# Performance work log

Measured on AMD Instinct MI355X. Metric: run time of the kernel, lower is better.

The kernel has to match this reference:

```python
import jax, jax.numpy as jnp
import numpy as np

B, T, C = 4, 4096, 1024   # batch, seq_len, n_embd
HS = 128                  # tamanho_cabeca (head size)


def setup_inputs() -> dict:
    key = jax.random.key(0)
    kx, kq, kk, kv = jax.random.split(key, 4)
    scale = 0.02
    return {
        "x": jax.random.normal(kx, (B, T, C), dtype=jnp.float32),
        "Wq": jax.random.normal(kq, (C, HS), dtype=jnp.float32) * scale,
        "Wk": jax.random.normal(kk, (C, HS), dtype=jnp.float32) * scale,
        "Wv": jax.random.normal(kv, (C, HS), dtype=jnp.float32) * scale,
    }


def reference(x, Wq, Wk, Wv):
    # Single-head causal self-attention, faithful to the torch Head module.
    _, Tn, Cn = x.shape
    q = jnp.einsum("btc,ch->bth", x, Wq)
    k = jnp.einsum("btc,ch->bth", x, Wk)
    v = jnp.einsum("btc,ch->bth", x, Wv)
    # NOTE: original scales by C**-0.5 (input embed dim), not head_size**-0.5.
    scores = jnp.einsum("bth,bsh->bts", q, k) * (Cn ** -0.5)
    causal = jnp.tril(jnp.ones((Tn, Tn), dtype=bool))  # [T, T]
    scores = jnp.where(causal, scores, -jnp.inf)
    probs = jax.nn.softmax(scores, axis=-1)
    return jnp.einsum("bts,bsh->bth", probs, v)
```

## Files before the change

kernel.cpp:

```cpp
#include <hip/hip_runtime.h>
#include <hip/hip_bf16.h>
#include <math.h>

typedef __attribute__((ext_vector_type(8))) short short8;
typedef __attribute__((ext_vector_type(4))) float f32x4;
typedef unsigned short ushort_t;

#define B_  4
#define T_  4096
#define C_  1024
#define HS_ 128

#define QSCALE 0.04508422002778011f

__device__ const unsigned char NS_[32] = {
    1,1,1,1,2,2,3,3,3,4,4,4,5,5,5,6,6,7,7,7,8,8,8,9,9,9,10,10,11,11,11,11};

__device__ __forceinline__ ushort_t f2bf(float f) {
    unsigned int u = __float_as_uint(f);
    u = (u + 0x7FFFu + ((u >> 16) & 1u)) >> 16;
    return (ushort_t)u;
}
__device__ __forceinline__ ushort_t f2bf_fast(float f) {
    return (ushort_t)((__float_as_uint(f) + 0x8000u) >> 16);
}
__device__ __forceinline__ float bf2f(ushort_t u) {
    return __uint_as_float(((unsigned)u) << 16);
}
__device__ __forceinline__ void async16(const void* g, void* l) {
    __builtin_amdgcn_global_load_lds(
        (const __attribute__((address_space(1))) unsigned int*)g,
        (__attribute__((address_space(3))) unsigned int*)l, 16, 0, 0);
}
__device__ __forceinline__ float exp2fast(float x) {
    return __builtin_amdgcn_exp2f(x);
}

__global__ __launch_bounds__(256) void wt_kernel(
    const float* __restrict__ Wq, const float* __restrict__ Wk,
    const float* __restrict__ Wv, ushort_t* __restrict__ WT3)
{
    __shared__ ushort_t sWT[128 * 68];
    const int blk = blockIdx.x, tid = threadIdx.x;
    const int m = blk >> 4, slab = blk & 15;
    const float* __restrict__ W = (m == 0) ? Wq : (m == 1) ? Wk : Wv;
    const int kc = slab * 64;
    const int r = tid >> 2, h0 = (tid & 3) * 32;
#pragma unroll
    for (int j = 0; j < 8; ++j) {
        float4 wv = *(const float4*)(W + (size_t)(kc + r) * 128 + h0 + j * 4);
        sWT[(h0 + j * 4 + 0) * 68 + r] = f2bf(wv.x);
        sWT[(h0 + j * 4 + 1) * 68 + r] = f2bf(wv.y);
        sWT[(h0 + j * 4 + 2) * 68 + r] = f2bf(wv.z);
        sWT[(h0 + j * 4 + 3) * 68 + r] = f2bf(wv.w);
    }
    __syncthreads();
#pragma unroll
    for (int j = 0; j < 4; ++j) {
        int d = j * 256 + tid;
        int h = d >> 3, c8 = d & 7;
        short8 o;
#pragma unroll
        for (int e = 0; e < 8; ++e) o[e] = (short)sWT[h * 68 + c8 * 8 + e];
        *(short8*)(WT3 + (size_t)(m * 128 + h) * 1024 + kc + c8 * 8) = o;
    }
}

__global__ __launch_bounds__(256, 3) void qkv_gemm(
    const float* __restrict__ x, const ushort_t* __restrict__ WT3,
    ushort_t* __restrict__ q, ushort_t* __restrict__ k,
    ushort_t* __restrict__ vT)
{
    __shared__ ushort_t smem[24576];

    const int tid  = threadIdx.x;
    const int t0   = blockIdx.x * 64;
    const int mm   = blockIdx.y;
    const int w    = tid >> 6, lane = tid & 63;
    const int quad = lane >> 4, l15 = lane & 15;

    const ushort_t* __restrict__ WTm = WT3 + (size_t)mm * (128 * 1024);

    const int arow = tid >> 3, ac = tid & 7;
    const float* __restrict__ gx = x + (size_t)(t0 + arow) * C_ + ac * 8;
    const int aswz = ((ac ^ (arow & 7)) * 8);

    const ushort_t* gB[4];
    int bdst[4];
#pragma unroll
    for (int j = 0; j < 4; ++j) {
        int d = j * 256 + tid, row = d >> 3, c = d & 7;
        gB[j] = WTm + (size_t)row * C_ + ((c ^ (row & 7)) * 8);
        bdst[j] = 4096 + d * 8;
    }

    f32x4 acc[8];
#pragma unroll
    for (int nt = 0; nt < 8; ++nt) acc[nt] = (f32x4)0.f;

    float4 ar[2][2];
#pragma unroll
    for (int p = 0; p < 2; ++p) {
        ar[p][0] = *(const float4*)(gx + (size_t)(p * 32) * C_);
        ar[p][1] = *(const float4*)(gx + (size_t)(p * 32) * C_ + 4);
    }
#pragma unroll
    for (int j = 0; j < 4; ++j) async16(gB[j], &smem[bdst[j]]);
#pragma unroll
    for (int p = 0; p < 2; ++p) {
        short8 sv;
        sv[0]=f2bf(ar[p][0].x); sv[1]=f2bf(ar[p][0].y);
        sv[2]=f2bf(ar[p][0].z); sv[3]=f2bf(ar[p][0].w);
        sv[4]=f2bf(ar[p][1].x); sv[5]=f2bf(ar[p][1].y);
        sv[6]=f2bf(ar[p][1].z); sv[7]=f2bf(ar[p][1].w);
        *(short8*)&smem[(p * 32 + arow) * 64 + aswz] = sv;
    }
    __syncthreads();

    const int arow_q = w * 16 + l15;
    for (int it = 0; it < 16; ++it) {
        const int buf = it & 1, nb = buf ^ 1;
        const bool more = (it < 15);
        if (more) {
            const int kc = (it + 1) * 64;
#pragma unroll
            for (int p = 0; p < 2; ++p) {
                ar[p][0] = *(const float4*)(gx + (size_t)(p * 32) * C_ + kc);
                ar[p][1] = *(const float4*)(gx + (size_t)(p * 32) * C_ + kc + 4);
            }
#pragma unroll
            for (int j = 0; j < 4; ++j)
                async16(gB[j] + kc, &smem[nb * 12288 + bdst[j]]);
        }
        const ushort_t* sA = &smem[buf * 12288];
        const ushort_t* sB = &smem[buf * 12288 + 4096];
#pragma unroll
        for (int kf = 0; kf < 2; ++kf) {
            short8 af = *(const short8*)&sA[arow_q * 64 + (((kf * 4 + quad) ^ (arow_q & 7)) * 8)];
#pragma unroll
            for (int nt = 0; nt < 8; ++nt) {
                int row = nt * 16 + l15;
                short8 bf = *(const short8*)&sB[row * 64 + (((kf * 4 + quad) ^ (row & 7)) * 8)];
                acc[nt] = __builtin_amdgcn_mfma_f32_16x16x32_bf16(af, bf, acc[nt], 0, 0, 0);
            }
        }
        if (more) {
#pragma unroll
            for (int p = 0; p < 2; ++p) {
                short8 sv;
                sv[0]=f2bf(ar[p][0].x); sv[1]=f2bf(ar[p][0].y);
                sv[2]=f2bf(ar[p][0].z); sv[3]=f2bf(ar[p][0].w);
                sv[4]=f2bf(ar[p][1].x); sv[5]=f2bf(ar[p][1].y);
                sv[6]=f2bf(ar[p][1].z); sv[7]=f2bf(ar[p][1].w);
                *(short8*)&smem[nb * 12288 + (p * 32 + arow) * 64 + aswz] = sv;
            }
        }
        __syncthreads();
    }

    if (mm < 2) {
        ushort_t* __restrict__ outp = (mm == 0) ? q : k;
        const float s = (mm == 0) ? QSCALE : 1.0f;
        ushort_t* sE = &smem[0];
#pragma unroll
        for (int nt = 0; nt < 8; ++nt)
#pragma unroll
            for (int rr = 0; rr < 4; ++rr)
                sE[(w * 16 + quad * 4 + rr) * 136 + nt * 16 + l15] =
                    f2bf(acc[nt][rr] * s);
        __syncthreads();
#pragma unroll
        for (int j = 0; j < 4; ++j) {
            int d = j * 256 + tid;
            int row = d >> 4, cs = d & 15;
            *(short8*)(outp + (size_t)(t0 + row) * HS_ + cs * 8) =
                *(const short8*)&sE[row * 136 + cs * 8];
        }
    } else {
        ushort_t* sT = &smem[0];
#pragma unroll
        for (int nt = 0; nt < 8; ++nt)
#pragma unroll
            for (int rr = 0; rr < 4; ++rr)
                sT[(w * 16 + quad * 4 + rr) * 132 + nt * 16 + l15] =
                    f2bf(acc[nt][rr]);
        __syncthreads();
        const int bb = t0 >> 12;
        const int tl = t0 & (T_ - 1);
#pragma unroll
        for (int j = 0; j < 4; ++j) {
            int d = j * 256 + tid;
            int h = d >> 3, t8 = d & 7;
            short8 o;
#pragma unroll
            for (int e = 0; e < 8; ++e)
                o[e] = (short)sT[(t8 * 8 + e) * 132 + h];
            *(short8*)(vT + ((size_t)(bb * HS_) + h) * T_ + tl + t8 * 8) = o;
        }
    }
}

__global__ __launch_bounds__(256, 3) void attn_seg(
    const ushort_t* __restrict__ q, const ushort_t* __restrict__ k,
    const ushort_t* __restrict__ vT, ushort_t* __restrict__ Opart,
    float* __restrict__ lseg)
{
    __shared__ ushort_t smem[23552];
    ushort_t* sKb = smem;
    ushort_t* sVb = smem + 8192;
    ushort_t* sP  = smem + 18432;

    const int tid  = threadIdx.x;
    const int bid  = blockIdx.x;
    const int bb   = (bid & 7) >> 1;
    const int seg  = ((bid >> 3) << 1) | (bid & 1);
    const int slot = bb * 192 + seg;
    int r_ = seg;
    int i = 0;
    while (r_ >= NS_[i]) { r_ -= NS_[i]; ++i; }
    const int s    = r_;
    const int ns   = NS_[i];
    const int qb   = i << 7;
    const int nkc  = (i + 1) << 2;
    const int c0   = (nkc * s) / ns;
    const int c1   = (nkc * (s + 1)) / ns;

    const int w    = tid >> 6, lane = tid & 63;
    const int quad = lane >> 4, l15 = lane & 15;
    const size_t bT = (size_t)bb << 12;

    const int kr0 = tid >> 4,          kc0 = tid & 15;
    const int kr1 = (tid + 256) >> 4,  kc1 = (tid + 256) & 15;
    const ushort_t* kp0 = k + (bT + (size_t)c0 * 32 + kr0) * HS_ + ((kc0 ^ (kr0 & 15)) * 8);
    const ushort_t* kp1 = k + (bT + (size_t)c0 * 32 + kr1) * HS_ + ((kc1 ^ (kr1 & 15)) * 8);
    const int vr0 = tid >> 2,          vc0 = tid & 3;
    const int vr1 = (tid + 256) >> 2,  vc1 = (tid + 256) & 3;
    const ushort_t* vp0 = vT + ((size_t)(bb * HS_) + vr0) * T_ + c0 * 32 + vc0 * 8;
    const ushort_t* vp1 = vT + ((size_t)(bb * HS_) + vr1) * T_ + c0 * 32 + vc1 * 8;
    const int vdst0 = vr0 * 40 + vc0 * 8;
    const int vdst1 = vr1 * 40 + vc1 * 8;

    short8 qf[2][4];
#pragma unroll
    for (int mt = 0; mt < 2; ++mt)
#pragma unroll
        for (int kf = 0; kf < 4; ++kf)
            qf[mt][kf] = *(const short8*)(
                q + (bT + qb + w * 32 + mt * 16 + l15) * HS_ + kf * 32 + quad * 8);

    f32x4 O[2][8];
    f32x4 O_l[2];
#pragma unroll
    for (int mt = 0; mt < 2; ++mt) {
        O_l[mt] = (f32x4)0.f;
#pragma unroll
        for (int nt = 0; nt < 8; ++nt) O[mt][nt] = (f32x4)0.f;
    }
    short8 ones;
#pragma unroll
    for (int e = 0; e < 8; ++e) ones[e] = (short)0x3F80;

    {
        short8 v0 = *(const short8*)vp0;
        short8 v1 = *(const short8*)vp1;
        async16(kp0, sKb + tid * 8);
        async16(kp1, sKb + (tid + 256) * 8);
        kp0 += 32 * HS_; kp1 += 32 * HS_; vp0 += 32; vp1 += 32;
        *(short8*)(sVb + vdst0) = v0;
        *(short8*)(sVb + vdst1) = v1;
    }
    __syncthreads();

    for (int c = c0; c < c1; ++c) {
        const int buf = (c - c0) & 1, nb = buf ^ 1;
        const int kb = c << 5;
        const bool more = (c + 1 < c1);
        short8 pv0, pv1;
        if (more) {
            pv0 = *(const short8*)vp0;
            pv1 = *(const short8*)vp1;
            async16(kp0, sKb + nb * 4096 + tid * 8);
            async16(kp1, sKb + nb * 4096 + (tid + 256) * 8);
            kp0 += 32 * HS_; kp1 += 32 * HS_; vp0 += 32; vp1 += 32;
        }
        const ushort_t* sK = sKb + buf * 4096;
        const ushort_t* sV = sVb + buf * 5120;

        f32x4 S[2][2];
        S[0][0] = (f32x4)0.f; S[0][1] = (f32x4)0.f;
        S[1][0] = (f32x4)0.f; S[1][1] = (f32x4)0.f;
#pragma unroll
        for (int nt = 0; nt < 2; ++nt) {
            int row = nt * 16 + l15;
#pragma unroll
            for (int kf = 0; kf < 4; ++kf) {
                short8 bf = *(const short8*)&sK[row * 128 + (((kf * 4 + quad) ^ l15) * 8)];
                S[0][nt] = __builtin_amdgcn_mfma_f32_16x16x32_bf16(qf[0][kf], bf, S[0][nt], 0, 0, 0);
                S[1][nt] = __builtin_amdgcn_mfma_f32_16x16x32_bf16(qf[1][kf], bf, S[1][nt], 0, 0, 0);
            }
        }
        if (kb + 31 > qb + w * 32) {
#pragma unroll
            for (int mt = 0; mt < 2; ++mt)
#pragma unroll
                for (int nt = 0; nt < 2; ++nt)
#pragma unroll
                    for (int rr = 0; rr < 4; ++rr)
                        if (kb + nt * 16 + l15 > qb + w * 32 + mt * 16 + quad * 4 + rr)
                            S[mt][nt][rr] = -1e30f;
        }
#pragma unroll
        for (int mt = 0; mt < 2; ++mt)
#pragma unroll
            for (int nt = 0; nt < 2; ++nt)
#pragma unroll
                for (int rr = 0; rr < 4; ++rr)
                    sP[w * 1280 + (mt * 16 + quad * 4 + rr) * 40 + nt * 16 + l15] =
                        f2bf_fast(exp2fast(S[mt][nt][rr]));
#pragma unroll
        for (int mt = 0; mt < 2; ++mt) {
            short8 pf = *(short8*)&sP[w * 1280 + (mt * 16 + l15) * 40 + quad * 8];
            O_l[mt] = __builtin_amdgcn_mfma_f32_16x16x32_bf16(pf, ones, O_l[mt], 0, 0, 0);
#pragma unroll
            for (int nt = 0; nt < 8; ++nt) {
                short8 vf = *(const short8*)&sV[(nt * 16 + l15) * 40 + quad * 8];
                O[mt][nt] = __builtin_amdgcn_mfma_f32_16x16x32_bf16(pf, vf, O[mt][nt], 0, 0, 0);
            }
        }
        if (more) {
            *(short8*)(sVb + nb * 5120 + vdst0) = pv0;
            *(short8*)(sVb + nb * 5120 + vdst1) = pv1;
        }
        __syncthreads();
    }

    ushort_t* sE = smem;
#pragma unroll
    for (int mt = 0; mt < 2; ++mt)
#pragma unroll
        for (int nt = 0; nt < 8; ++nt)
#pragma unroll
            for (int rr = 0; rr < 4; ++rr)
                sE[(w * 32 + mt * 16 + quad * 4 + rr) * 136 + nt * 16 + l15] =
                    f2bf(O[mt][nt][rr]);
    if (l15 == 0)
#pragma unroll
        for (int mt = 0; mt < 2; ++mt)
#pragma unroll
            for (int rr = 0; rr < 4; ++rr)
                lseg[slot * 128 + w * 32 + mt * 16 + quad * 4 + rr] = O_l[mt][rr];
    __syncthreads();
#pragma unroll
    for (int j = 0; j < 8; ++j) {
        int d = j * 256 + tid;
        int row = d >> 4, cs = d & 15;
        *(short8*)(Opart + (size_t)slot * 16384 + row * 128 + cs * 8) =
            *(const short8*)&sE[row * 136 + cs * 8];
    }
}

__global__ __launch_bounds__(256) void combine_kernel(
    const ushort_t* __restrict__ Opart, const float* __restrict__ lseg,
    float* __restrict__ out)
{
    const int blk  = blockIdx.x;
    const int tile = blk >> 2, rg = blk & 3;
    const int i    = tile & 31;
    int sb = (tile >> 5) * 192;
    for (int j = 0; j < i; ++j) sb += NS_[j];
    const int ns  = NS_[i];
    const int row = rg * 32 + (threadIdx.x >> 3);
    const int col = (threadIdx.x & 7) * 16;

    float den = 0.f;
    float acc[16];
#pragma unroll
    for (int e = 0; e < 16; ++e) acc[e] = 0.f;
    for (int s = 0; s < ns; ++s) {
        const int slot = sb + s;
        den += lseg[slot * 128 + row];
        const ushort_t* op = Opart + (size_t)slot * 16384 + row * 128 + col;
        short8 a = *(const short8*)op;
        short8 b = *(const short8*)(op + 8);
#pragma unroll
        for (int e = 0; e < 8; ++e) {
            acc[e]     += bf2f((ushort_t)a[e]);
            acc[8 + e] += bf2f((ushort_t)b[e]);
        }
    }
    const float inv = 1.0f / den;
    float* op = out + ((size_t)tile * 128 + row) * 128 + col;
#pragma unroll
    for (int g = 0; g < 4; ++g) {
        float4 v = make_float4(acc[g*4] * inv, acc[g*4+1] * inv,
                               acc[g*4+2] * inv, acc[g*4+3] * inv);
        *(float4*)(op + g * 4) = v;
    }
}

extern "C" void kernel_launch(void* const* d_in, const int* in_sizes, int n_in,
                              void* d_out, int out_size, void* d_ws, size_t ws_size,
                              hipStream_t stream)
{
    const float* x  = (const float*)d_in[0];
    const float* Wq = (const float*)d_in[1];
    const float* Wk = (const float*)d_in[2];
    const float* Wv = (const float*)d_in[3];
    float* out = (float*)d_out;

    ushort_t* WT3 = (ushort_t*)d_ws;
    ushort_t* q   = WT3 + 393216;
    ushort_t* k   = q + 2097152;
    ushort_t* vT  = k + 2097152;
    ushort_t* Opart = vT + 2097152;
    float* lseg   = (float*)(Opart + 768 * 16384);

    wt_kernel<<<48, 256, 0, stream>>>(Wq, Wk, Wv, WT3);
    qkv_gemm<<<dim3(256, 3), 256, 0, stream>>>(x, WT3, q, k, vT);
    attn_seg<<<768, 256, 0, stream>>>(q, k, vT, Opart, lseg);
    combine_kernel<<<512, 256, 0, stream>>>(Opart, lseg, out);
}
```

Measured before the change: 167.7 us.

## Fuse Q/K/V projections into one block computing all 384 output columns

Each QKV GEMM block now computes all three projections (384 columns) for its 64-row tile instead of launching three separate blocks per tile. As a result, x is read from global memory and converted to bf16 once rather than three times. Each wave owns 96 output columns across all 64 rows, holding a 4x6 MFMA accumulator tile. This needs about 112 KB of dynamic shared memory and allows one block per CU, so the grid drops to 256 blocks, trading occupancy and parallelism for less redundant x traffic.

```diff
diff --git a/kernel.cpp b/kernel.cpp
--- a/kernel.cpp
+++ b/kernel.cpp
@@ -66,37 +66,36 @@
     }
 }
 
-__global__ __launch_bounds__(256, 3) void qkv_gemm(
+__global__ __launch_bounds__(256, 1) void qkv_gemm(
     const float* __restrict__ x, const ushort_t* __restrict__ WT3,
     ushort_t* __restrict__ q, ushort_t* __restrict__ k,
     ushort_t* __restrict__ vT)
 {
-    __shared__ ushort_t smem[24576];
+    extern __shared__ ushort_t smem[];
 
     const int tid  = threadIdx.x;
     const int t0   = blockIdx.x * 64;
-    const int mm   = blockIdx.y;
     const int w    = tid >> 6, lane = tid & 63;
     const int quad = lane >> 4, l15 = lane & 15;
-
-    const ushort_t* __restrict__ WTm = WT3 + (size_t)mm * (128 * 1024);
 
     const int arow = tid >> 3, ac = tid & 7;
     const float* __restrict__ gx = x + (size_t)(t0 + arow) * C_ + ac * 8;
     const int aswz = ((ac ^ (arow & 7)) * 8);
 
-    const ushort_t* gB[4];
-    int bdst[4];
-#pragma unroll
-    for (int j = 0; j < 4; ++j) {
+    const ushort_t* gB[12];
+    int bdst[12];
+#pragma unroll
+    for (int j = 0; j < 12; ++j) {
         int d = j * 256 + tid, row = d >> 3, c = d & 7;
-        gB[j] = WTm + (size_t)row * C_ + ((c ^ (row & 7)) * 8);
+        gB[j] = WT3 + (size_t)row * C_ + ((c ^ (row & 7)) * 8);
         bdst[j] = 4096 + d * 8;
     }
 
-    f32x4 acc[8];
-#pragma unroll
-    for (int nt = 0; nt < 8; ++nt) acc[nt] = (f32x4)0.f;
+    f32x4 acc[4][6];
+#pragma unroll
+    for (int mt = 0; mt < 4; ++mt)
+#pragma unroll
+        for (int nt = 0; nt < 6; ++nt) acc[mt][nt] = (f32x4)0.f;
 
     float4 ar[2][2];
 #pragma unroll
@@ -105,7 +104,7 @@
         ar[p][1] = *(const float4*)(gx + (size_t)(p * 32) * C_ + 4);
     }
 #pragma unroll
-    for (int j = 0; j < 4; ++j) async16(gB[j], &smem[bdst[j]]);
+    for (int j = 0; j < 12; ++j) async16(gB[j], &smem[bdst[j]]);
 #pragma unroll
     for (int p = 0; p < 2; ++p) {
         short8 sv;
@@ -117,7 +116,6 @@
     }
     __syncthreads();
 
-    const int arow_q = w * 16 + l15;
     for (int it = 0; it < 16; ++it) {
         const int buf = it & 1, nb = buf ^ 1;
         const bool more = (it < 15);
@@ -129,19 +127,26 @@
                 ar[p][1] = *(const float4*)(gx + (size_t)(p * 32) * C_ + kc + 4);
             }
 #pragma unroll
-            for (int j = 0; j < 4; ++j)
-                async16(gB[j] + kc, &smem[nb * 12288 + bdst[j]]);
-        }
-        const ushort_t* sA = &smem[buf * 12288];
-        const ushort_t* sB = &smem[buf * 12288 + 4096];
+            for (int j = 0; j < 12; ++j)
+                async16(gB[j] + kc, &smem[nb * 28672 + bdst[j]]);
+        }
+        const ushort_t* sA = &smem[buf * 28672];
+        const ushort_t* sB = &smem[buf * 28672 + 4096];
 #pragma unroll
         for (int kf = 0; kf < 2; ++kf) {
-            short8 af = *(const short8*)&sA[arow_q * 64 + (((kf * 4 + quad) ^ (arow_q & 7)) * 8)];
-#pragma unroll
-            for (int nt = 0; nt < 8; ++nt) {
-                int row = nt * 16 + l15;
+            short8 af[4];
+#pragma unroll
+            for (int mt = 0; mt < 4; ++mt) {
+                int ar_ = mt * 16 + l15;
+                af[mt] = *(const short8*)&sA[ar_ * 64 + (((kf * 4 + quad) ^ (ar_ & 7)) * 8)];
+            }
+#pragma unroll
+            for (int nt = 0; nt < 6; ++nt) {
+                int row = w * 96 + nt * 16 + l15;
                 short8 bf = *(const short8*)&sB[row * 64 + (((kf * 4 + quad) ^ (row & 7)) * 8)];
-                acc[nt] = __builtin_amdgcn_mfma_f32_16x16x32_bf16(af, bf, acc[nt], 0, 0, 0);
+#pragma unroll
+                for (int mt = 0; mt < 4; ++mt)
+                    acc[mt][nt] = __builtin_amdgcn_mfma_f32_16x16x32_bf16(af[mt], bf, acc[mt][nt], 0, 0, 0);
             }
         }
         if (more) {
@@ -152,39 +157,50 @@
                 sv[2]=f2bf(ar[p][0].z); sv[3]=f2bf(ar[p][0].w);
                 sv[4]=f2bf(ar[p][1].x); sv[5]=f2bf(ar[p][1].y);
                 sv[6]=f2bf(ar[p][1].z); sv[7]=f2bf(ar[p][1].w);
-                *(short8*)&smem[nb * 12288 + (p * 32 + arow) * 64 + aswz] = sv;
+                *(short8*)&smem[nb * 28672 + (p * 32 + arow) * 64 + aswz] = sv;
             }
         }
         __syncthreads();
     }
 
-    if (mm < 2) {
-        ushort_t* __restrict__ outp = (mm == 0) ? q : k;
-        const float s = (mm == 0) ? QSCALE : 1.0f;
-        ushort_t* sE = &smem[0];
-#pragma unroll
-        for (int nt = 0; nt < 8; ++nt)
-#pragma unroll
-            for (int rr = 0; rr < 4; ++rr)
-                sE[(w * 16 + quad * 4 + rr) * 136 + nt * 16 + l15] =
-                    f2bf(acc[nt][rr] * s);
-        __syncthreads();
-#pragma unroll
-        for (int j = 0; j < 4; ++j) {
-            int d = j * 256 + tid;
-            int row = d >> 4, cs = d & 15;
-            *(short8*)(outp + (size_t)(t0 + row) * HS_ + cs * 8) =
-                *(const short8*)&sE[row * 136 + cs * 8];
-        }
-    } else {
-        ushort_t* sT = &smem[0];
-#pragma unroll
-        for (int nt = 0; nt < 8; ++nt)
-#pragma unroll
-            for (int rr = 0; rr < 4; ++rr)
-                sT[(w * 16 + quad * 4 + rr) * 132 + nt * 16 + l15] =
-                    f2bf(acc[nt][rr]);
-        __syncthreads();
+    ushort_t* sE = smem;
+    ushort_t* sT = smem + 64 * 264;
+#pragma unroll
+    for (int nt = 0; nt < 6; ++nt) {
+        const int gc = w * 96 + nt * 16;
+        if (gc < 256) {
+            const float s = (gc < 128) ? QSCALE : 1.0f;
+#pragma unroll
+            for (int mt = 0; mt < 4; ++mt)
+#pragma unroll
+                for (int rr = 0; rr < 4; ++rr)
+                    sE[(mt * 16 + quad * 4 + rr) * 264 + gc + l15] =
+                        f2bf(acc[mt][nt][rr] * s);
+        } else {
+#pragma unroll
+            for (int mt = 0; mt < 4; ++mt)
+#pragma unroll
+                for (int rr = 0; rr < 4; ++rr)
+                    sT[(mt * 16 + quad * 4 + rr) * 132 + (gc - 256) + l15] =
+                        f2bf(acc[mt][nt][rr]);
+        }
+    }
+    __syncthreads();
+#pragma unroll
+    for (int j = 0; j < 4; ++j) {
+        int d = j * 256 + tid;
+        int row = d >> 4, cs = d & 15;
+        *(short8*)(q + (size_t)(t0 + row) * HS_ + cs * 8) =
+            *(const short8*)&sE[row * 264 + cs * 8];
+    }
+#pragma unroll
+    for (int j = 0; j < 4; ++j) {
+        int d = j * 256 + tid;
+        int row = d >> 4, cs = d & 15;
+        *(short8*)(k + (size_t)(t0 + row) * HS_ + cs * 8) =
+            *(const short8*)&sE[row * 264 + 128 + cs * 8];
+    }
+    {
         const int bb = t0 >> 12;
         const int tl = t0 & (T_ - 1);
 #pragma unroll
@@ -416,7 +432,7 @@
     float* lseg   = (float*)(Opart + 768 * 16384);
 
     wt_kernel<<<48, 256, 0, stream>>>(Wq, Wk, Wv, WT3);
-    qkv_gemm<<<dim3(256, 3), 256, 0, stream>>>(x, WT3, q, k, vT);
+    qkv_gemm<<<256, 256, 114688, stream>>>(x, WT3, q, k, vT);
     attn_seg<<<768, 256, 0, stream>>>(q, k, vT, Opart, lseg);
     combine_kernel<<<512, 256, 0, stream>>>(Opart, lseg, out);
 }
```

Result: no change. 167.3 us (-0.2%).
